# Performance work log

Measured on AMD Instinct MI355X. Metric: run time of the kernel, lower is better.

## Reference

```python
import jax, jax.numpy as jnp
import numpy as np

B, S, H = 8, 4096, 2048
HINT, WS, STRIDE = 4, 16, 8
MLP_H = 64


def _window_starts():
    # Mirrors the torch loop: break when the window is shorter than window_size//2.
    starts = []
    for s in range(0, S, STRIDE):
        e = min(s + WS, S)
        if e - s < WS // 2:
            break
        starts.append(s)
    return np.asarray(starts, dtype=np.int32)  # [W] = [512]


def setup_inputs() -> dict:
    key = jax.random.key(0)
    k1, k2, k3, k4, k5 = jax.random.split(key, 5)
    return {
        "hidden_states": jax.random.normal(k1, (B, S, H), jnp.float32),
        "attention_mask": jax.random.randint(k2, (B, S), 0, 2).astype(jnp.int32),
        "hint_features": jax.random.normal(k3, (B, S, HINT), jnp.float32),
        "W1": jax.random.normal(k4, (H + HINT, MLP_H), jnp.float32) * 0.02,
        "b1": jnp.zeros((MLP_H,), jnp.float32),
        "W2": jax.random.normal(k5, (MLP_H, 1), jnp.float32) * 0.02,
        "b2": jnp.zeros((1,), jnp.float32),
    }


def reference(hidden_states, attention_mask, hint_features, W1, b1, W2, b2):
    starts = jnp.asarray(_window_starts())               # [W]
    idx = starts[:, None] + jnp.arange(WS)               # [W, ws]
    pos_valid = (idx < S).astype(jnp.float32)            # [W, ws]  (pads past seq end)
    idxc = jnp.minimum(idx, S - 1)

    # [B, W, ws] combined attention + in-bounds mask
    mask = attention_mask[:, idxc].astype(jnp.float32) * pos_valid[None]
    denom = jnp.clip(jnp.sum(mask, axis=-1, keepdims=True), 1.0, None)  # [B, W, 1]

    # Gather overlapping windows once, pool with a single einsum each.
    win_h = hidden_states[:, idxc]                        # [B, W, ws, H]
    win_f = hint_features[:, idxc]                        # [B, W, ws, HINT]
    pooled_h = jnp.einsum('bwk,bwkh->bwh', mask, win_h) / denom
    pooled_f = jnp.einsum('bwk,bwkh->bwh', mask, win_f) / denom
    pooled = jnp.concatenate([pooled_h, pooled_f], axis=-1)  # [B, W, H+HINT]

    # MLP (dropout is identity at inference); torch GELU default = exact erf.
    h = jax.nn.gelu(pooled @ W1 + b1, approximate=False)
    window_logits = (h @ W2 + b2)[..., 0]                 # [B, W]
    window_mask = (jnp.sum(mask, axis=-1) > 0).astype(jnp.float32)  # [B, W]
    return window_logits, window_mask
```

## Files before the change

kernel.cpp:

```cpp
#include <hip/hip_runtime.h>
#include <math.h>

#define B_      8
#define S_      4096
#define H_      2048
#define HINT_   4
#define WS_     16
#define STRIDE_ 8
#define MLPH_   64
#define NW_     512
#define WPB_    8
#define ROWS_   72
#define KT_     68
#define KPAD_   2176
#define LDK_    2184
#define NT_     4
#define PLD_    66

typedef float  floatx4 __attribute__((ext_vector_type(4)));
typedef short  shortx8 __attribute__((ext_vector_type(8)));

__device__ __forceinline__ unsigned short f2b(float x) {
    unsigned u = __float_as_uint(x);
    u += 0x7FFFu + ((u >> 16) & 1u);
    return (unsigned short)(u >> 16);
}

__global__ void prep_w1(const float* __restrict__ W1, unsigned short* __restrict__ W1B) {
    const int blk  = blockIdx.x;
    const int nt   = blk / KT_;
    const int kt   = blk % KT_;
    const int lane = threadIdx.x;
    const int n     = nt * 16 + (lane & 15);
    const int kbase = kt * 32 + (lane >> 4) * 8;
    unsigned short tmp[8];
#pragma unroll
    for (int j = 0; j < 8; ++j) {
        const int k = kbase + j;
        const float v = (k < (H_ + HINT_)) ? W1[(size_t)k * MLPH_ + n] : 0.0f;
        tmp[j] = f2b(v);
    }
    *(uint4*)(W1B + (((size_t)nt * KT_ + kt) * 64 + lane) * 8) = *(const uint4*)tmp;
}

__global__ __launch_bounds__(512, 6) void wbh_kernel(
    const float* __restrict__ hidden,
    const int*   __restrict__ amask,
    const float* __restrict__ hintf,
    const float* __restrict__ b1,
    const float* __restrict__ W2,
    const float* __restrict__ b2,
    const unsigned short* __restrict__ W1B,
    float* __restrict__ out)
{
    __shared__ unsigned short pooledLds[WPB_ * LDK_];
    __shared__ float amLds[ROWS_];
    __shared__ float rinvLds[WPB_];
    __shared__ float partLds[WPB_ * PLD_];

    const int tid = threadIdx.x;
    const int bid = blockIdx.x;
    const int gid   = (bid & 7) * 64 + (bid >> 3);
    const int b     = gid >> 6;
    const int chunk = gid & 63;
    const int w0    = chunk * WPB_;
    const int s0    = chunk * (WPB_ * STRIDE_);

    if (tid < 8 * 62) {
        const int row = tid / 62, cc = tid % 62;
        *(unsigned*)&pooledLds[row * LDK_ + 2052 + cc * 2] = 0u;
    }
    if (tid < ROWS_) {
        const int p = s0 + tid;
        amLds[tid] = (p < S_) ? (float)amask[b * S_ + p] : 0.0f;
    }
    __syncthreads();

    if (tid < WPB_) {
        float s = 0.f;
#pragma unroll
        for (int k = 0; k < WS_; ++k) s += amLds[tid * STRIDE_ + k];
        rinvLds[tid] = 1.0f / fmaxf(s, 1.0f);
        out[(size_t)(B_ * NW_) + (size_t)b * NW_ + w0 + tid] = (s > 0.f) ? 1.0f : 0.0f;
    }
    __syncthreads();

    const int c0 = tid * 4;
    const float* rowBase = hidden + ((size_t)b * S_ + s0) * H_ + c0;

    floatx4 prev = (floatx4){0.f, 0.f, 0.f, 0.f};
#pragma unroll
    for (int g = 0; g <= WPB_; ++g) {
        float am[STRIDE_];
        const float* ptr[STRIDE_];
#pragma unroll
        for (int k = 0; k < STRIDE_; ++k) {
            const int rr = g * STRIDE_ + k;
            am[k]  = amLds[rr];
            ptr[k] = (am[k] != 0.0f) ? (rowBase + (size_t)rr * H_) : rowBase;
        }
        floatx4 v[STRIDE_];
#pragma unroll
        for (int k = 0; k < STRIDE_; ++k) v[k] = *(const floatx4*)ptr[k];

        floatx4 cur = (floatx4){0.f, 0.f, 0.f, 0.f};
#pragma unroll
        for (int k = 0; k < STRIDE_; ++k) {
            cur.x = fmaf(am[k], v[k].x, cur.x);
            cur.y = fmaf(am[k], v[k].y, cur.y);
            cur.z = fmaf(am[k], v[k].z, cur.z);
            cur.w = fmaf(am[k], v[k].w, cur.w);
        }
        if (g >= 1) {
            const int w = g - 1;
            const floatx4 s = prev + cur;
            const float r = rinvLds[w];
            unsigned short q[4];
            q[0] = f2b(s.x * r); q[1] = f2b(s.y * r);
            q[2] = f2b(s.z * r); q[3] = f2b(s.w * r);
            *(uint2*)(&pooledLds[w * LDK_ + c0]) = *(const uint2*)q;
        }
        prev = cur;
    }

    if (tid < WPB_ * HINT_) {
        const int w = tid >> 2, hc = tid & 3;
        float s = 0.f;
#pragma unroll
        for (int k = 0; k < WS_; ++k) {
            const int rr = w * STRIDE_ + k;
            const float amv = amLds[rr];
            float hv = 0.f;
            if (amv != 0.0f)
                hv = hintf[((size_t)b * S_ + (s0 + rr)) * HINT_ + hc];
            s += amv * hv;
        }
        pooledLds[w * LDK_ + H_ + hc] = f2b(s * rinvLds[w]);
    }
    __syncthreads();

    const int wid  = tid >> 6;
    const int lane = tid & 63;
    if (wid < NT_) {
        floatx4 dacc = (floatx4){0.f, 0.f, 0.f, 0.f};
        const unsigned short* aBase = pooledLds + (lane & 7) * LDK_ + (lane >> 4) * 8;
        const unsigned short* bBase = W1B + ((size_t)wid * KT_ * 64 + lane) * 8;
#pragma unroll 4
        for (int kt = 0; kt < KT_; ++kt) {
            const shortx8 af = *(const shortx8*)(aBase + kt * 32);
            const shortx8 bf = *(const shortx8*)(bBase + (size_t)kt * 64 * 8);
            dacc = __builtin_amdgcn_mfma_f32_16x16x32_bf16(af, bf, dacc, 0, 0, 0);
        }
        if (lane < 32) {
            const int m0 = (lane >> 4) * 4;
            const int j  = wid * 16 + (lane & 15);
#pragma unroll
            for (int r = 0; r < 4; ++r)
                partLds[(m0 + r) * PLD_ + j] = dacc[r];
        }
    }
    __syncthreads();

    {
        const int m = tid >> 6;
        const int j = tid & 63;
        const float a = partLds[m * PLD_ + j] + b1[j];
        float g = 0.5f * a * (1.0f + erff(a * 0.70710678118654752f)) * W2[j];
#pragma unroll
        for (int off = 32; off > 0; off >>= 1) g += __shfl_down(g, off, 64);
        if (j == 0) out[(size_t)b * NW_ + w0 + m] = g + b2[0];
    }
}

extern "C" void kernel_launch(void* const* d_in, const int* in_sizes, int n_in,
                              void* d_out, int out_size, void* d_ws, size_t ws_size,
                              hipStream_t stream) {
    const float* hidden = (const float*)d_in[0];
    const int*   amask  = (const int*)d_in[1];
    const float* hintf  = (const float*)d_in[2];
    const float* W1     = (const float*)d_in[3];
    const float* b1     = (const float*)d_in[4];
    const float* W2     = (const float*)d_in[5];
    const float* b2     = (const float*)d_in[6];
    float* out          = (float*)d_out;

    unsigned short* W1B = (unsigned short*)d_ws;

    prep_w1<<<NT_ * KT_, 64, 0, stream>>>(W1, W1B);
    wbh_kernel<<<B_ * (NW_ / WPB_), 512, 0, stream>>>(
        hidden, amask, hintf, b1, W2, b2, W1B, out);
}
```

Baseline: 349.2 us.

## Halve windows per block and give each thread two column vectors

Each block now handles 4 windows instead of 8, with 256 threads instead of 512, so the grid doubles to 1024 blocks and the batch-major block swizzle is removed. Each thread loads and pools two float4 columns 1024 apart, which puts more independent loads in flight per thread. All four waves now run the bf16 MFMA MLP, using only 4 of the 16 A-rows. The trade-off is a larger overlapping-row halo per block (40 rows for 4 windows instead of 72 for 8), twice as many per-block reads of W1B, and more wasted MFMA rows.

```diff
diff --git a/kernel.cpp b/kernel.cpp
--- a/kernel.cpp
+++ b/kernel.cpp
@@ -9,8 +9,8 @@
 #define STRIDE_ 8
 #define MLPH_   64
 #define NW_     512
-#define WPB_    8
-#define ROWS_   72
+#define WPB_    4
+#define ROWS_   40
 #define KT_     68
 #define KPAD_   2176
 #define LDK_    2184
@@ -43,7 +43,7 @@
     *(uint4*)(W1B + (((size_t)nt * KT_ + kt) * 64 + lane) * 8) = *(const uint4*)tmp;
 }
 
-__global__ __launch_bounds__(512, 6) void wbh_kernel(
+__global__ __launch_bounds__(256) void wbh_kernel(
     const float* __restrict__ hidden,
     const int*   __restrict__ amask,
     const float* __restrict__ hintf,
@@ -60,13 +60,12 @@
 
     const int tid = threadIdx.x;
     const int bid = blockIdx.x;
-    const int gid   = (bid & 7) * 64 + (bid >> 3);
-    const int b     = gid >> 6;
-    const int chunk = gid & 63;
+    const int b     = bid >> 7;
+    const int chunk = bid & 127;
     const int w0    = chunk * WPB_;
     const int s0    = chunk * (WPB_ * STRIDE_);
 
-    if (tid < 8 * 62) {
+    if (tid < WPB_ * 62) {
         const int row = tid / 62, cc = tid % 62;
         *(unsigned*)&pooledLds[row * LDK_ + 2052 + cc * 2] = 0u;
     }
@@ -88,39 +87,49 @@
     const int c0 = tid * 4;
     const float* rowBase = hidden + ((size_t)b * S_ + s0) * H_ + c0;
 
-    floatx4 prev = (floatx4){0.f, 0.f, 0.f, 0.f};
+    floatx4 prevA = (floatx4){0.f,0.f,0.f,0.f}, prevB = prevA;
 #pragma unroll
     for (int g = 0; g <= WPB_; ++g) {
-        float am[STRIDE_];
-        const float* ptr[STRIDE_];
-#pragma unroll
-        for (int k = 0; k < STRIDE_; ++k) {
-            const int rr = g * STRIDE_ + k;
-            am[k]  = amLds[rr];
-            ptr[k] = (am[k] != 0.0f) ? (rowBase + (size_t)rr * H_) : rowBase;
-        }
-        floatx4 v[STRIDE_];
-#pragma unroll
-        for (int k = 0; k < STRIDE_; ++k) v[k] = *(const floatx4*)ptr[k];
-
-        floatx4 cur = (floatx4){0.f, 0.f, 0.f, 0.f};
-#pragma unroll
-        for (int k = 0; k < STRIDE_; ++k) {
-            cur.x = fmaf(am[k], v[k].x, cur.x);
-            cur.y = fmaf(am[k], v[k].y, cur.y);
-            cur.z = fmaf(am[k], v[k].z, cur.z);
-            cur.w = fmaf(am[k], v[k].w, cur.w);
+        floatx4 curA = (floatx4){0.f,0.f,0.f,0.f}, curB = curA;
+#pragma unroll
+        for (int kk = 0; kk < 2; ++kk) {
+            float am[4];
+            const float* p[4];
+#pragma unroll
+            for (int k2 = 0; k2 < 4; ++k2) {
+                const int rr = g * STRIDE_ + kk * 4 + k2;
+                am[k2] = amLds[rr];
+                p[k2]  = (am[k2] != 0.0f) ? (rowBase + (size_t)rr * H_) : rowBase;
+            }
+            floatx4 vA[4], vB[4];
+#pragma unroll
+            for (int k2 = 0; k2 < 4; ++k2) {
+                vA[k2] = *(const floatx4*)(p[k2]);
+                vB[k2] = *(const floatx4*)(p[k2] + 1024);
+            }
+#pragma unroll
+            for (int k2 = 0; k2 < 4; ++k2) {
+                curA.x = fmaf(am[k2], vA[k2].x, curA.x);
+                curA.y = fmaf(am[k2], vA[k2].y, curA.y);
+                curA.z = fmaf(am[k2], vA[k2].z, curA.z);
+                curA.w = fmaf(am[k2], vA[k2].w, curA.w);
+                curB.x = fmaf(am[k2], vB[k2].x, curB.x);
+                curB.y = fmaf(am[k2], vB[k2].y, curB.y);
+                curB.z = fmaf(am[k2], vB[k2].z, curB.z);
+                curB.w = fmaf(am[k2], vB[k2].w, curB.w);
+            }
         }
         if (g >= 1) {
             const int w = g - 1;
-            const floatx4 s = prev + cur;
             const float r = rinvLds[w];
-            unsigned short q[4];
-            q[0] = f2b(s.x * r); q[1] = f2b(s.y * r);
-            q[2] = f2b(s.z * r); q[3] = f2b(s.w * r);
-            *(uint2*)(&pooledLds[w * LDK_ + c0]) = *(const uint2*)q;
-        }
-        prev = cur;
+            const floatx4 sA = prevA + curA, sB = prevB + curB;
+            unsigned short qA[4], qB[4];
+            qA[0]=f2b(sA.x*r); qA[1]=f2b(sA.y*r); qA[2]=f2b(sA.z*r); qA[3]=f2b(sA.w*r);
+            qB[0]=f2b(sB.x*r); qB[1]=f2b(sB.y*r); qB[2]=f2b(sB.z*r); qB[3]=f2b(sB.w*r);
+            *(uint2*)(&pooledLds[w * LDK_ + c0])        = *(const uint2*)qA;
+            *(uint2*)(&pooledLds[w * LDK_ + c0 + 1024]) = *(const uint2*)qB;
+        }
+        prevA = curA; prevB = curB;
     }
 
     if (tid < WPB_ * HINT_) {
@@ -141,9 +150,9 @@
 
     const int wid  = tid >> 6;
     const int lane = tid & 63;
-    if (wid < NT_) {
+    {
         floatx4 dacc = (floatx4){0.f, 0.f, 0.f, 0.f};
-        const unsigned short* aBase = pooledLds + (lane & 7) * LDK_ + (lane >> 4) * 8;
+        const unsigned short* aBase = pooledLds + (lane & 3) * LDK_ + (lane >> 4) * 8;
         const unsigned short* bBase = W1B + ((size_t)wid * KT_ * 64 + lane) * 8;
 #pragma unroll 4
         for (int kt = 0; kt < KT_; ++kt) {
@@ -151,12 +160,11 @@
             const shortx8 bf = *(const shortx8*)(bBase + (size_t)kt * 64 * 8);
             dacc = __builtin_amdgcn_mfma_f32_16x16x32_bf16(af, bf, dacc, 0, 0, 0);
         }
-        if (lane < 32) {
-            const int m0 = (lane >> 4) * 4;
-            const int j  = wid * 16 + (lane & 15);
+        if (lane < 16) {
+            const int j = wid * 16 + lane;
 #pragma unroll
             for (int r = 0; r < 4; ++r)
-                partLds[(m0 + r) * PLD_ + j] = dacc[r];
+                partLds[r * PLD_ + j] = dacc[r];
         }
     }
     __syncthreads();
@@ -187,6 +195,6 @@
     unsigned short* W1B = (unsigned short*)d_ws;
 
     prep_w1<<<NT_ * KT_, 64, 0, stream>>>(W1, W1B);
-    wbh_kernel<<<B_ * (NW_ / WPB_), 512, 0, stream>>>(
+    wbh_kernel<<<B_ * (NW_ / WPB_), 256, 0, stream>>>(
         hidden, amask, hintf, b1, W2, b2, W1B, out);
 }
```

Result: no change. 352.3 us (+0.9%).
